# Optimization experiments

Measured on AMD Instinct MI355X. Metric: run time of the kernel, lower is better.

The kernel has to match this reference:

```python
import jax, jax.numpy as jnp
import numpy as np

H = 16        # num_attention_heads
HS = 128      # head_size
ROT = 32      # rotary_ndims (partial RoPE, NeoX rotary_pct=0.25)
BASE = 10000.0


def _rope_cache(seq_len):
    inv_freq = 1.0 / (BASE ** (jnp.arange(0, ROT, 2, dtype=jnp.float32) / ROT))
    t = jnp.arange(seq_len, dtype=jnp.float32)
    freqs = jnp.outer(t, inv_freq)                      # [s, ROT/2]
    emb = jnp.concatenate([freqs, freqs], axis=-1)      # [s, ROT]
    return jnp.cos(emb), jnp.sin(emb)


def _rotate_half(x):
    x1, x2 = jnp.split(x, 2, axis=-1)
    return jnp.concatenate([-x2, x1], axis=-1)


def setup_inputs() -> dict:
    key = jax.random.key(0)
    k1, k2, k3 = jax.random.split(key, 3)
    B, S, D = 2, 2048, 2048
    hidden_states = jax.random.normal(k1, (B, S, D), dtype=jnp.float32)
    position_ids = jnp.broadcast_to(jnp.arange(S, dtype=jnp.int64 if jax.config.jax_enable_x64 else jnp.int32), (B, S))
    W_qkv = jax.random.normal(k2, (D, 3 * H * HS), dtype=jnp.float32) * 0.02
    b_qkv = jnp.zeros((3 * H * HS,), dtype=jnp.float32)
    W_dense = jax.random.normal(k3, (H * HS, D), dtype=jnp.float32) * 0.02
    b_dense = jnp.zeros((D,), dtype=jnp.float32)
    return {"hidden_states": hidden_states, "position_ids": position_ids,
            "W_qkv": W_qkv, "b_qkv": b_qkv, "W_dense": W_dense, "b_dense": b_dense}


def reference(hidden_states, position_ids, W_qkv, b_qkv, W_dense, b_dense):
    B, S, D = hidden_states.shape
    # fused QKV projection, NeoX layout: [b, s, h, 3*hs]
    qkv = (hidden_states @ W_qkv + b_qkv).reshape(B, S, H, 3 * HS)
    q = qkv[..., :HS]            # [b, s, h, hs]
    k = qkv[..., HS:2 * HS]
    v = qkv[..., 2 * HS:]

    # partial rotary embedding on first ROT dims
    cos, sin = _rope_cache(S)                       # [s, ROT]
    cos = cos[position_ids][:, :, None, :]          # [b, s, 1, ROT]
    sin = sin[position_ids][:, :, None, :]
    q_rot, q_pass = q[..., :ROT], q[..., ROT:]
    k_rot, k_pass = k[..., :ROT], k[..., ROT:]
    q_rot = q_rot * cos + _rotate_half(q_rot) * sin
    k_rot = k_rot * cos + _rotate_half(k_rot) * sin
    q = jnp.concatenate([q_rot, q_pass], axis=-1)
    k = jnp.concatenate([k_rot, k_pass], axis=-1)

    # scaled dot-product attention (no mask, as in the source SDPA call)
    scale = 1.0 / jnp.sqrt(jnp.asarray(HS, dtype=q.dtype))
    scores = jnp.einsum('bqhd,bkhd->bhqk', q, k) * scale   # [b, h, s, s]
    attn = jax.nn.softmax(scores, axis=-1)
    out = jnp.einsum('bhqk,bkhd->bqhd', attn, v)            # [b, s, h, hs]
    out = out.reshape(B, S, H * HS)                         # 'b h d n -> b d (h n)'
    return out @ W_dense + b_dense
```

## Files before the change

kernel.cpp:

```cpp
#include <hip/hip_runtime.h>

typedef short bf16x8 __attribute__((ext_vector_type(8)));
typedef float f32x4 __attribute__((ext_vector_type(4)));

#define S_LEN 2048
#define NHEAD 16
#define HSZ 128

__device__ __forceinline__ float bf2f(ushort u) {
    union { unsigned int i; float f; } x; x.i = ((unsigned int)u) << 16; return x.f;
}
__device__ __forceinline__ ushort f2bf(float f) {
    union { float f; unsigned int i; } x; x.f = f;
    unsigned int r = (x.i + 0x7FFFu + ((x.i >> 16) & 1u)) >> 16;
    return (ushort)r;
}

__device__ __forceinline__ void gload16(const ushort* g, ushort* l) {
    __builtin_amdgcn_global_load_lds(
        (const __attribute__((address_space(1))) unsigned int*)g,
        (__attribute__((address_space(3))) unsigned int*)l,
        16, 0, 0);
}

#define BAR()   asm volatile("s_barrier" ::: "memory")
#define LGKM0() asm volatile("s_waitcnt lgkmcnt(0)" ::: "memory")

__global__ void cast_kernel(const float* __restrict__ in, ushort* __restrict__ out, int n4) {
    int i = blockIdx.x * 256 + threadIdx.x;
    if (i >= n4) return;
    float4 v = ((const float4*)in)[i];
    ushort4 r;
    r.x = f2bf(v.x); r.y = f2bf(v.y); r.z = f2bf(v.z); r.w = f2bf(v.w);
    ((ushort4*)out)[i] = r;
}

__global__ void transpose_cast(const float* __restrict__ W, ushort* __restrict__ WT,
                               int K, int N) {
    __shared__ float tile[32][33];
    int n = blockIdx.x * 32 + threadIdx.x;
    #pragma unroll
    for (int j = 0; j < 32; j += 8) {
        int k = blockIdx.y * 32 + threadIdx.y + j;
        tile[threadIdx.y + j][threadIdx.x] = W[(size_t)k * N + n];
    }
    __syncthreads();
    int k2 = blockIdx.y * 32 + threadIdx.x;
    #pragma unroll
    for (int j = 0; j < 32; j += 8) {
        int n2 = blockIdx.x * 32 + threadIdx.y + j;
        WT[(size_t)n2 * K + k2] = f2bf(tile[threadIdx.x][threadIdx.y + j]);
    }
}

template <int EPI>
__global__ __launch_bounds__(512, 2) void gemm256(
    const ushort* __restrict__ A, const ushort* __restrict__ Bt,
    const float* __restrict__ bias, float* __restrict__ Cout, int Kdim, int Ndim,
    ushort* __restrict__ q_out, ushort* __restrict__ k_out, ushort* __restrict__ v_out) {
    __shared__ __align__(16) ushort lds[65536];
    const int tid = threadIdx.x;
    const int m0 = blockIdx.y * 256, n0 = blockIdx.x * 256;
    const int lane = tid & 63, wid = tid >> 6;
    const int wm = wid >> 2, wn = wid & 3;
    const int lm = lane & 15, quad = lane >> 4;
    const int cs = (quad ^ ((lm >> 1) & 3)) * 8;
    const int aOff = wm * 8192 + lm * 32 + cs;
    const int bOff = 16384 + (wn >> 1) * 8192 + (wn & 1) * 2048 + lm * 32 + cs;
    const int srow = tid >> 2;
    const int xs8 = ((tid & 3) ^ ((tid >> 3) & 3)) * 8;
    const ushort* pAs = A  + (size_t)(m0 + srow) * Kdim + xs8;
    const ushort* pBs = Bt + (size_t)(n0 + srow) * Kdim + xs8;
    const size_t hK = (size_t)128 * Kdim;
    const int sw = wid * 512;

    f32x4 acc[8][4];
    #pragma unroll
    for (int i = 0; i < 8; ++i)
        #pragma unroll
        for (int j = 0; j < 4; ++j) acc[i][j] = (f32x4){0.f, 0.f, 0.f, 0.f};

    const int T = Kdim >> 6;

    auto stageB = [&](int t) {
        ushort* b = lds + (t & 1) * 32768 + 16384 + sw;
        const ushort* g = pBs + (size_t)t * 64;
        gload16(g,            b);
        gload16(g + 32,       b + 4096);
        gload16(g + hK,       b + 8192);
        gload16(g + hK + 32,  b + 12288);
    };
    auto stageA = [&](int t) {
        ushort* b = lds + (t & 1) * 32768 + sw;
        const ushort* g = pAs + (size_t)t * 64;
        gload16(g,            b);
        gload16(g + 32,       b + 4096);
        gload16(g + hK,       b + 8192);
        gload16(g + hK + 32,  b + 12288);
    };

    stageB(0); stageA(0); stageB(1); stageA(1);
    asm volatile("s_waitcnt vmcnt(8)" ::: "memory");
    BAR();

    for (int t = 0; t < T; ++t) {
        const ushort* la = lds + (t & 1) * 32768 + aOff;
        const ushort* lb = lds + (t & 1) * 32768 + bOff;
        const bool pf = (t + 2 < T);

        bf16x8 afL[4][2], bfL[2][2];
        #pragma unroll
        for (int mt = 0; mt < 4; ++mt)
            #pragma unroll
            for (int ks = 0; ks < 2; ++ks)
                afL[mt][ks] = *(const bf16x8*)(la + ks * 4096 + mt * 512);
        #pragma unroll
        for (int nt = 0; nt < 2; ++nt)
            #pragma unroll
            for (int ks = 0; ks < 2; ++ks)
                bfL[nt][ks] = *(const bf16x8*)(lb + ks * 4096 + nt * 512);
        BAR(); LGKM0();
        __builtin_amdgcn_s_setprio(1);
        #pragma unroll
        for (int mt = 0; mt < 4; ++mt)
            #pragma unroll
            for (int nt = 0; nt < 2; ++nt) {
                acc[mt][nt] = __builtin_amdgcn_mfma_f32_16x16x32_bf16(afL[mt][0], bfL[nt][0], acc[mt][nt], 0, 0, 0);
                acc[mt][nt] = __builtin_amdgcn_mfma_f32_16x16x32_bf16(afL[mt][1], bfL[nt][1], acc[mt][nt], 0, 0, 0);
            }
        __builtin_amdgcn_s_setprio(0);
        BAR();

        bf16x8 bfH[2][2];
        #pragma unroll
        for (int nt = 0; nt < 2; ++nt)
            #pragma unroll
            for (int ks = 0; ks < 2; ++ks)
                bfH[nt][ks] = *(const bf16x8*)(lb + ks * 4096 + (nt + 2) * 512);
        BAR(); LGKM0();
        __builtin_amdgcn_s_setprio(1);
        #pragma unroll
        for (int mt = 0; mt < 4; ++mt)
            #pragma unroll
            for (int nt = 0; nt < 2; ++nt) {
                acc[mt][nt + 2] = __builtin_amdgcn_mfma_f32_16x16x32_bf16(afL[mt][0], bfH[nt][0], acc[mt][nt + 2], 0, 0, 0);
                acc[mt][nt + 2] = __builtin_amdgcn_mfma_f32_16x16x32_bf16(afL[mt][1], bfH[nt][1], acc[mt][nt + 2], 0, 0, 0);
            }
        __builtin_amdgcn_s_setprio(0);
        BAR();

        bf16x8 afH[4][2];
        #pragma unroll
        for (int mt = 0; mt < 4; ++mt)
            #pragma unroll
            for (int ks = 0; ks < 2; ++ks)
                afH[mt][ks] = *(const bf16x8*)(la + ks * 4096 + (mt + 4) * 512);
        if (pf) stageB(t + 2);
        BAR(); LGKM0();
        __builtin_amdgcn_s_setprio(1);
        #pragma unroll
        for (int mt = 0; mt < 4; ++mt)
            #pragma unroll
            for (int nt = 0; nt < 2; ++nt) {
                acc[mt + 4][nt] = __builtin_amdgcn_mfma_f32_16x16x32_bf16(afH[mt][0], bfL[nt][0], acc[mt + 4][nt], 0, 0, 0);
                acc[mt + 4][nt] = __builtin_amdgcn_mfma_f32_16x16x32_bf16(afH[mt][1], bfL[nt][1], acc[mt + 4][nt], 0, 0, 0);
            }
        __builtin_amdgcn_s_setprio(0);
        BAR();

        if (pf) stageA(t + 2);
        BAR();
        __builtin_amdgcn_s_setprio(1);
        #pragma unroll
        for (int mt = 0; mt < 4; ++mt)
            #pragma unroll
            for (int nt = 0; nt < 2; ++nt) {
                acc[mt + 4][nt + 2] = __builtin_amdgcn_mfma_f32_16x16x32_bf16(afH[mt][0], bfH[nt][0], acc[mt + 4][nt + 2], 0, 0, 0);
                acc[mt + 4][nt + 2] = __builtin_amdgcn_mfma_f32_16x16x32_bf16(afH[mt][1], bfH[nt][1], acc[mt + 4][nt + 2], 0, 0, 0);
            }
        __builtin_amdgcn_s_setprio(0);
        if (pf) asm volatile("s_waitcnt vmcnt(8)" ::: "memory");
        else    asm volatile("s_waitcnt vmcnt(0)" ::: "memory");
        BAR();
    }

    #pragma unroll
    for (int mt = 0; mt < 8; ++mt) {
        #pragma unroll
        for (int nt = 0; nt < 4; ++nt) {
            f32x4 c = acc[mt][nt];
            int gn = n0 + wn * 64 + nt * 16 + lm;
            float bv = bias[gn];
            #pragma unroll
            for (int i = 0; i < 4; ++i) {
                int gm = m0 + wm * 128 + mt * 16 + quad * 4 + i;
                float v = c[i] + bv;
                if (EPI == 0) {
                    int h = gn / 384, r = gn - h * 384;
                    int tt = r >> 7, d = r & 127;
                    int b = gm >> 11, s = gm & 2047;
                    ushort bb = f2bf(v);
                    if (tt == 0) {
                        q_out[((size_t)(b * NHEAD + h) * S_LEN + s) * HSZ + d] = bb;
                    } else if (tt == 1) {
                        k_out[((size_t)(b * NHEAD + h) * S_LEN + s) * HSZ + d] = bb;
                    } else {
                        v_out[((size_t)(b * NHEAD + h) * HSZ + d) * S_LEN + s] = bb;
                    }
                } else {
                    Cout[(size_t)gm * Ndim + gn] = v;
                }
            }
        }
    }
}

template <int EPI>
__global__ __launch_bounds__(256) void gemm128(
    const ushort* __restrict__ A, const ushort* __restrict__ Bt,
    const float* __restrict__ bias, float* __restrict__ Cout, int Kdim, int Ndim,
    ushort* __restrict__ q_out, ushort* __restrict__ k_out, ushort* __restrict__ v_out) {
    __shared__ __align__(16) ushort lA[2][128 * 32];
    __shared__ __align__(16) ushort lB[2][128 * 32];
    const int tid = threadIdx.x;
    const int m0 = blockIdx.y * 128, n0 = blockIdx.x * 128;
    const int lane = tid & 63, wid = tid >> 6;
    const int wm = wid >> 1, wn = wid & 1, lm = lane & 15, quad = lane >> 4;
    const int srow = tid >> 2;
    const int gc = (tid & 3) ^ ((tid >> 3) & 3);
    const int wb8 = (wid << 6) * 8;
    const int cs = (quad ^ ((lm >> 1) & 3)) * 8;

    const ushort* pA = A  + (size_t)(m0 + srow) * Kdim + gc * 8;
    const ushort* pB = Bt + (size_t)(n0 + srow) * Kdim + gc * 8;
    const size_t rhalf = (size_t)64 * Kdim;

    const int fA = (wm * 64 + lm) * 32;
    const int fB = (wn * 64 + lm) * 32;

    f32x4 acc[16];
    #pragma unroll
    for (int i = 0; i < 16; ++i) acc[i] = (f32x4){0.f, 0.f, 0.f, 0.f};

    const int T = Kdim >> 5;
    gload16(pA,         lA[0] + wb8);
    gload16(pA + rhalf, lA[0] + 2048 + wb8);
    gload16(pB,         lB[0] + wb8);
    gload16(pB + rhalf, lB[0] + 2048 + wb8);
    pA += 32; pB += 32;

    for (int t = 0; t < T; ++t) {
        __syncthreads();
        const ushort* la = lA[t & 1];
        const ushort* lb = lB[t & 1];
        if (t + 1 < T) {
            ushort* da = lA[(t + 1) & 1];
            ushort* db = lB[(t + 1) & 1];
            gload16(pA,         da + wb8);
            gload16(pA + rhalf, da + 2048 + wb8);
            gload16(pB,         db + wb8);
            gload16(pB + rhalf, db + 2048 + wb8);
            pA += 32; pB += 32;
        }
        bf16x8 af[4], bfr[4];
        #pragma unroll
        for (int t4 = 0; t4 < 4; ++t4) {
            af[t4]  = *(const bf16x8*)(la + fA + t4 * 512 + cs);
            bfr[t4] = *(const bf16x8*)(lb + fB + t4 * 512 + cs);
        }
        #pragma unroll
        for (int mt = 0; mt < 4; ++mt)
            #pragma unroll
            for (int nt = 0; nt < 4; ++nt)
                acc[mt * 4 + nt] = __builtin_amdgcn_mfma_f32_16x16x32_bf16(
                    af[mt], bfr[nt], acc[mt * 4 + nt], 0, 0, 0);
    }

    #pragma unroll
    for (int mt = 0; mt < 4; ++mt) {
        #pragma unroll
        for (int nt = 0; nt < 4; ++nt) {
            f32x4 c = acc[mt * 4 + nt];
            int gn = n0 + wn * 64 + nt * 16 + lm;
            float bv = bias[gn];
            #pragma unroll
            for (int i = 0; i < 4; ++i) {
                int gm = m0 + wm * 64 + mt * 16 + quad * 4 + i;
                float v = c[i] + bv;
                if (EPI == 0) {
                    int h = gn / 384, r = gn - h * 384;
                    int t = r >> 7, d = r & 127;
                    int b = gm >> 11, s = gm & 2047;
                    ushort bb = f2bf(v);
                    if (t == 0) {
                        q_out[((size_t)(b * NHEAD + h) * S_LEN + s) * HSZ + d] = bb;
                    } else if (t == 1) {
                        k_out[((size_t)(b * NHEAD + h) * S_LEN + s) * HSZ + d] = bb;
                    } else {
                        v_out[((size_t)(b * NHEAD + h) * HSZ + d) * S_LEN + s] = bb;
                    }
                } else {
                    Cout[(size_t)gm * Ndim + gn] = v;
                }
            }
        }
    }
}

__global__ void rope_kernel(ushort* __restrict__ Qr, ushort* __restrict__ Kr,
                            const int* __restrict__ pos_ids) {
    int idx = blockIdx.x * 256 + threadIdx.x;
    int j = idx & 15;
    int row = idx >> 4;
    int s = row & 2047;
    int bh = row >> 11;
    int b = bh >> 4;
    int pos = pos_ids[b * S_LEN + s];
    float inv = exp2f((float)j * -0.8304820237218405f);
    float th = (float)pos * inv;
    float sn, c;
    sincosf(th, &sn, &c);
    size_t base = (size_t)row * HSZ;
    {
        float x1 = bf2f(Qr[base + j]), x2 = bf2f(Qr[base + j + 16]);
        Qr[base + j]      = f2bf(x1 * c - x2 * sn);
        Qr[base + j + 16] = f2bf(x2 * c + x1 * sn);
    }
    {
        float x1 = bf2f(Kr[base + j]), x2 = bf2f(Kr[base + j + 16]);
        Kr[base + j]      = f2bf(x1 * c - x2 * sn);
        Kr[base + j + 16] = f2bf(x2 * c + x1 * sn);
    }
}

__global__ __launch_bounds__(256, 2) void attn_mfma(
    const ushort* __restrict__ Q, const ushort* __restrict__ K,
    const ushort* __restrict__ Vt, ushort* __restrict__ O) {
    __shared__ __align__(16) ushort lQ[128 * 136];
    __shared__ __align__(16) ushort lK[2][32 * 128];
    __shared__ __align__(16) ushort lVt[2][128 * 32];
    __shared__ __align__(16) ushort lP[4 * 32 * 40];

    const int tid = threadIdx.x;
    const int wid = tid >> 6, lane = tid & 63;
    const int L = lane & 15, quad = lane >> 4;
    const int bh = blockIdx.y;
    const int q0 = blockIdx.x * 128;
    const int wq0 = wid * 32;
    const size_t base = (size_t)bh * S_LEN * HSZ;
    const ushort* Qb = Q + base + (size_t)q0 * HSZ;
    const ushort* Kb = K + base;
    const ushort* Vb = Vt + base;
    ushort* lPw = lP + wid * (32 * 40);

    #pragma unroll
    for (int p = 0; p < 8; ++p) {
        int idx = tid + p * 256;
        int row = idx >> 4, ch = idx & 15;
        uint4 v = ((const uint4*)Qb)[idx];
        *(uint4*)(lQ + row * 136 + ch * 8) = v;
    }
    __syncthreads();

    bf16x8 qf[2][4];
    #pragma unroll
    for (int qs = 0; qs < 2; ++qs)
        #pragma unroll
        for (int dc = 0; dc < 4; ++dc)
            qf[qs][dc] = *(const bf16x8*)(lQ + (wq0 + qs * 16 + L) * 136 + dc * 32 + quad * 8);

    int kx[4];
    #pragma unroll
    for (int dc = 0; dc < 4; ++dc) kx[dc] = (((dc * 4 + quad) ^ (L & 7))) * 8;
    const int vx = (quad ^ ((L >> 1) & 3)) * 8;

    const int li0 = tid, li1 = tid + 256;
    const int ub0 = ((tid & 192)) * 8, ub1 = ((tid & 192) + 256) * 8;
    const int kr0 = li0 >> 4, kg0 = (li0 & 15) ^ (kr0 & 7);
    const int kr1 = li1 >> 4, kg1 = (li1 & 15) ^ (kr1 & 7);
    const int vd0 = li0 >> 2, vg0 = (li0 & 3) ^ ((vd0 >> 1) & 3);
    const int vd1 = li1 >> 2, vg1 = (li1 & 3) ^ ((vd1 >> 1) & 3);

    f32x4 acc_o[8][2];
    #pragma unroll
    for (int dt = 0; dt < 8; ++dt)
        #pragma unroll
        for (int qs = 0; qs < 2; ++qs) acc_o[dt][qs] = (f32x4){0.f, 0.f, 0.f, 0.f};
    float lacc[2] = {0.f, 0.f};
    const float scale = 0.08838834764831845f;
    const float SHIFT = 12.0f;

    {
        gload16(Kb + (size_t)kr0 * 128 + kg0 * 8, lK[0] + ub0);
        gload16(Kb + (size_t)kr1 * 128 + kg1 * 8, lK[0] + ub1);
        gload16(Vb + (size_t)vd0 * 2048 + vg0 * 8, lVt[0] + ub0);
        gload16(Vb + (size_t)vd1 * 2048 + vg1 * 8, lVt[0] + ub1);
    }

    for (int kt = 0; kt < S_LEN / 32; ++kt) {
        __syncthreads();
        const int cur = kt & 1;
        const ushort* lKc = lK[cur];
        const ushort* lVc = lVt[cur];
        if (kt + 1 < S_LEN / 32) {
            ushort* dK = lK[cur ^ 1];
            ushort* dV = lVt[cur ^ 1];
            int kb = (kt + 1) * 32;
            gload16(Kb + (size_t)(kb + kr0) * 128 + kg0 * 8, dK + ub0);
            gload16(Kb + (size_t)(kb + kr1) * 128 + kg1 * 8, dK + ub1);
            gload16(Vb + (size_t)vd0 * 2048 + kb + vg0 * 8, dV + ub0);
            gload16(Vb + (size_t)vd1 * 2048 + kb + vg1 * 8, dV + ub1);
        }

        f32x4 sa[2][2];
        #pragma unroll
        for (int t = 0; t < 2; ++t)
            #pragma unroll
            for (int qs = 0; qs < 2; ++qs) sa[t][qs] = (f32x4){0.f, 0.f, 0.f, 0.f};
        #pragma unroll
        for (int t = 0; t < 2; ++t)
            #pragma unroll
            for (int dc = 0; dc < 4; ++dc) {
                bf16x8 kf = *(const bf16x8*)(lKc + (t * 16 + L) * 128 + kx[dc]);
                sa[t][0] = __builtin_amdgcn_mfma_f32_16x16x32_bf16(kf, qf[0][dc], sa[t][0], 0, 0, 0);
                sa[t][1] = __builtin_amdgcn_mfma_f32_16x16x32_bf16(kf, qf[1][dc], sa[t][1], 0, 0, 0);
            }

        #pragma unroll
        for (int t = 0; t < 2; ++t)
            #pragma unroll
            for (int qs = 0; qs < 2; ++qs) {
                #pragma unroll
                for (int r = 0; r < 4; ++r) {
                    float pv = __expf(fmaf(sa[t][qs][r], scale, -SHIFT));
                    lacc[qs] += pv;
                    sa[t][qs][r] = pv;
                }
                ushort4 u;
                u.x = f2bf(sa[t][qs][0]);
                u.y = f2bf(sa[t][qs][1]);
                u.z = f2bf(sa[t][qs][2]);
                u.w = f2bf(sa[t][qs][3]);
                *(ushort4*)(lPw + (qs * 16 + L) * 40 + t * 16 + quad * 4) = u;
            }
        __asm__ volatile("s_waitcnt lgkmcnt(0)" ::: "memory");

        bf16x8 pf0 = *(const bf16x8*)(lPw + L * 40 + quad * 8);
        bf16x8 pf1 = *(const bf16x8*)(lPw + (16 + L) * 40 + quad * 8);
        #pragma unroll
        for (int dt = 0; dt < 8; ++dt) {
            bf16x8 vf = *(const bf16x8*)(lVc + (dt * 16 + L) * 32 + vx);
            acc_o[dt][0] = __builtin_amdgcn_mfma_f32_16x16x32_bf16(vf, pf0, acc_o[dt][0], 0, 0, 0);
            acc_o[dt][1] = __builtin_amdgcn_mfma_f32_16x16x32_bf16(vf, pf1, acc_o[dt][1], 0, 0, 0);
        }
    }

    const int b = bh >> 4, h = bh & 15;
    #pragma unroll
    for (int qs = 0; qs < 2; ++qs) {
        float l = lacc[qs];
        l += __shfl_xor(l, 16);
        l += __shfl_xor(l, 32);
        float inv = 1.f / l;
        size_t row = ((size_t)(b * S_LEN + q0 + wq0 + qs * 16 + L)) * (NHEAD * HSZ) + h * HSZ;
        #pragma unroll
        for (int dt = 0; dt < 8; ++dt) {
            ushort4 u;
            u.x = f2bf(acc_o[dt][qs][0] * inv);
            u.y = f2bf(acc_o[dt][qs][1] * inv);
            u.z = f2bf(acc_o[dt][qs][2] * inv);
            u.w = f2bf(acc_o[dt][qs][3] * inv);
            *(ushort4*)(O + row + dt * 16 + quad * 4) = u;
        }
    }
}

extern "C" void kernel_launch(void* const* d_in, const int* in_sizes, int n_in,
                              void* d_out, int out_size, void* d_ws, size_t ws_size,
                              hipStream_t stream) {
    const float* hidden = (const float*)d_in[0];
    const int*   pos    = (const int*)d_in[1];
    const float* Wqkv   = (const float*)d_in[2];
    const float* bqkv   = (const float*)d_in[3];
    const float* Wd     = (const float*)d_in[4];
    const float* bd     = (const float*)d_in[5];

    char* ws = (char*)d_ws;
    ushort* hA  = (ushort*)ws;
    ushort* WqT = (ushort*)(ws + 16777216ull);
    ushort* WdT = (ushort*)(ws + 41943040ull);
    ushort* Qb  = (ushort*)(ws + 50331648ull);
    ushort* Kb  = (ushort*)(ws + 67108864ull);
    ushort* Vb  = (ushort*)(ws + 83886080ull);

    cast_kernel<<<dim3(8192), dim3(256), 0, stream>>>(hidden, hA, 2097152);
    transpose_cast<<<dim3(192, 64), dim3(32, 8), 0, stream>>>(Wqkv, WqT, 2048, 6144);
    transpose_cast<<<dim3(64, 64), dim3(32, 8), 0, stream>>>(Wd, WdT, 2048, 2048);

    gemm256<0><<<dim3(24, 16), dim3(512), 0, stream>>>(hA, WqT, bqkv, nullptr, 2048, 6144,
                                                       Qb, Kb, Vb);
    rope_kernel<<<dim3(4096), dim3(256), 0, stream>>>(Qb, Kb, pos);

    ushort* Obuf = hA;
    attn_mfma<<<dim3(16, 32), dim3(256), 0, stream>>>(Qb, Kb, Vb, Obuf);

    gemm128<1><<<dim3(16, 32), dim3(256), 0, stream>>>(Obuf, WdT, bd, (float*)d_out,
                                                       2048, 2048, nullptr, nullptr, nullptr);
}
```

Measured before the change: 440.0 us.

## Enlarge attention block to 256 queries and 64-key tiles with 8 waves

The attention kernel now runs 512 threads (8 waves) per block, covering 256 query rows, and streams K/V in 64-key tiles instead of 32. The V^T tile uses a new 8-way XOR swizzle, and the P·V step is split into two 32-key halves that reuse the per-wave P staging buffer. The goal is to halve K/V global and LDS traffic per query and the number of barriers per key. The cost is much more LDS per block and 256 blocks, about one per CU, so occupancy drops. The 512-thread launch bound also puts more pressure on registers, which could cause spills.

```diff
diff --git a/kernel.cpp b/kernel.cpp
--- a/kernel.cpp
+++ b/kernel.cpp
@@ -333,19 +333,19 @@
     }
 }
 
-__global__ __launch_bounds__(256, 2) void attn_mfma(
+__global__ __launch_bounds__(512, 2) void attn_mfma(
     const ushort* __restrict__ Q, const ushort* __restrict__ K,
     const ushort* __restrict__ Vt, ushort* __restrict__ O) {
-    __shared__ __align__(16) ushort lQ[128 * 136];
-    __shared__ __align__(16) ushort lK[2][32 * 128];
-    __shared__ __align__(16) ushort lVt[2][128 * 32];
-    __shared__ __align__(16) ushort lP[4 * 32 * 40];
+    __shared__ __align__(16) ushort lQ[256 * 136];
+    __shared__ __align__(16) ushort lK[2][64 * 128];
+    __shared__ __align__(16) ushort lVt[2][128 * 64];
+    __shared__ __align__(16) ushort lP[8 * 32 * 40];
 
     const int tid = threadIdx.x;
     const int wid = tid >> 6, lane = tid & 63;
     const int L = lane & 15, quad = lane >> 4;
     const int bh = blockIdx.y;
-    const int q0 = blockIdx.x * 128;
+    const int q0 = blockIdx.x * 256;
     const int wq0 = wid * 32;
     const size_t base = (size_t)bh * S_LEN * HSZ;
     const ushort* Qb = Q + base + (size_t)q0 * HSZ;
@@ -355,7 +355,7 @@
 
     #pragma unroll
     for (int p = 0; p < 8; ++p) {
-        int idx = tid + p * 256;
+        int idx = tid + p * 512;
         int row = idx >> 4, ch = idx & 15;
         uint4 v = ((const uint4*)Qb)[idx];
         *(uint4*)(lQ + row * 136 + ch * 8) = v;
@@ -371,15 +371,15 @@
 
     int kx[4];
     #pragma unroll
-    for (int dc = 0; dc < 4; ++dc) kx[dc] = (((dc * 4 + quad) ^ (L & 7))) * 8;
-    const int vx = (quad ^ ((L >> 1) & 3)) * 8;
-
-    const int li0 = tid, li1 = tid + 256;
-    const int ub0 = ((tid & 192)) * 8, ub1 = ((tid & 192) + 256) * 8;
-    const int kr0 = li0 >> 4, kg0 = (li0 & 15) ^ (kr0 & 7);
-    const int kr1 = li1 >> 4, kg1 = (li1 & 15) ^ (kr1 & 7);
-    const int vd0 = li0 >> 2, vg0 = (li0 & 3) ^ ((vd0 >> 1) & 3);
-    const int vd1 = li1 >> 2, vg1 = (li1 & 3) ^ ((vd1 >> 1) & 3);
+    for (int dc = 0; dc < 4; ++dc) kx[dc] = ((dc * 4 + quad) ^ (L & 7)) * 8;
+    const int vx0 = ((0 * 4 + quad) ^ (L & 7)) * 8;
+    const int vx1 = ((1 * 4 + quad) ^ (L & 7)) * 8;
+
+    const int ub  = (tid & 0x1C0) * 8;
+    const int kr0 = tid >> 4,  kg0 = (tid & 15) ^ (kr0 & 7);
+    const int kr1 = kr0 + 32;
+    const int vd0 = tid >> 3,  vg0 = (tid & 7) ^ (vd0 & 7);
+    const int vd1 = vd0 + 64;
 
     f32x4 acc_o[8][2];
     #pragma unroll
@@ -391,34 +391,34 @@
     const float SHIFT = 12.0f;
 
     {
-        gload16(Kb + (size_t)kr0 * 128 + kg0 * 8, lK[0] + ub0);
-        gload16(Kb + (size_t)kr1 * 128 + kg1 * 8, lK[0] + ub1);
-        gload16(Vb + (size_t)vd0 * 2048 + vg0 * 8, lVt[0] + ub0);
-        gload16(Vb + (size_t)vd1 * 2048 + vg1 * 8, lVt[0] + ub1);
-    }
-
-    for (int kt = 0; kt < S_LEN / 32; ++kt) {
+        gload16(Kb + (size_t)kr0 * 128 + kg0 * 8, lK[0] + ub);
+        gload16(Kb + (size_t)kr1 * 128 + kg0 * 8, lK[0] + 4096 + ub);
+        gload16(Vb + (size_t)vd0 * 2048 + vg0 * 8, lVt[0] + ub);
+        gload16(Vb + (size_t)vd1 * 2048 + vg0 * 8, lVt[0] + 4096 + ub);
+    }
+
+    for (int kt = 0; kt < S_LEN / 64; ++kt) {
         __syncthreads();
         const int cur = kt & 1;
         const ushort* lKc = lK[cur];
         const ushort* lVc = lVt[cur];
-        if (kt + 1 < S_LEN / 32) {
+        if (kt + 1 < S_LEN / 64) {
             ushort* dK = lK[cur ^ 1];
             ushort* dV = lVt[cur ^ 1];
-            int kb = (kt + 1) * 32;
-            gload16(Kb + (size_t)(kb + kr0) * 128 + kg0 * 8, dK + ub0);
-            gload16(Kb + (size_t)(kb + kr1) * 128 + kg1 * 8, dK + ub1);
-            gload16(Vb + (size_t)vd0 * 2048 + kb + vg0 * 8, dV + ub0);
-            gload16(Vb + (size_t)vd1 * 2048 + kb + vg1 * 8, dV + ub1);
-        }
-
-        f32x4 sa[2][2];
-        #pragma unroll
-        for (int t = 0; t < 2; ++t)
+            int kb = (kt + 1) * 64;
+            gload16(Kb + (size_t)(kb + kr0) * 128 + kg0 * 8, dK + ub);
+            gload16(Kb + (size_t)(kb + kr1) * 128 + kg0 * 8, dK + 4096 + ub);
+            gload16(Vb + (size_t)vd0 * 2048 + kb + vg0 * 8, dV + ub);
+            gload16(Vb + (size_t)vd1 * 2048 + kb + vg0 * 8, dV + 4096 + ub);
+        }
+
+        f32x4 sa[4][2];
+        #pragma unroll
+        for (int t = 0; t < 4; ++t)
             #pragma unroll
             for (int qs = 0; qs < 2; ++qs) sa[t][qs] = (f32x4){0.f, 0.f, 0.f, 0.f};
         #pragma unroll
-        for (int t = 0; t < 2; ++t)
+        for (int t = 0; t < 4; ++t)
             #pragma unroll
             for (int dc = 0; dc < 4; ++dc) {
                 bf16x8 kf = *(const bf16x8*)(lKc + (t * 16 + L) * 128 + kx[dc]);
@@ -427,31 +427,36 @@
             }
 
         #pragma unroll
-        for (int t = 0; t < 2; ++t)
-            #pragma unroll
-            for (int qs = 0; qs < 2; ++qs) {
+        for (int h = 0; h < 2; ++h) {
+            #pragma unroll
+            for (int t2 = 0; t2 < 2; ++t2) {
+                int t = h * 2 + t2;
                 #pragma unroll
-                for (int r = 0; r < 4; ++r) {
-                    float pv = __expf(fmaf(sa[t][qs][r], scale, -SHIFT));
-                    lacc[qs] += pv;
-                    sa[t][qs][r] = pv;
+                for (int qs = 0; qs < 2; ++qs) {
+                    #pragma unroll
+                    for (int r = 0; r < 4; ++r) {
+                        float pv = __expf(fmaf(sa[t][qs][r], scale, -SHIFT));
+                        lacc[qs] += pv;
+                        sa[t][qs][r] = pv;
+                    }
+                    ushort4 u;
+                    u.x = f2bf(sa[t][qs][0]);
+                    u.y = f2bf(sa[t][qs][1]);
+                    u.z = f2bf(sa[t][qs][2]);
+                    u.w = f2bf(sa[t][qs][3]);
+                    *(ushort4*)(lPw + (qs * 16 + L) * 40 + t2 * 16 + quad * 4) = u;
                 }
-                ushort4 u;
-                u.x = f2bf(sa[t][qs][0]);
-                u.y = f2bf(sa[t][qs][1]);
-                u.z = f2bf(sa[t][qs][2]);
-                u.w = f2bf(sa[t][qs][3]);
-                *(ushort4*)(lPw + (qs * 16 + L) * 40 + t * 16 + quad * 4) = u;
-            }
-        __asm__ volatile("s_waitcnt lgkmcnt(0)" ::: "memory");
-
-        bf16x8 pf0 = *(const bf16x8*)(lPw + L * 40 + quad * 8);
-        bf16x8 pf1 = *(const bf16x8*)(lPw + (16 + L) * 40 + quad * 8);
-        #pragma unroll
-        for (int dt = 0; dt < 8; ++dt) {
-            bf16x8 vf = *(const bf16x8*)(lVc + (dt * 16 + L) * 32 + vx);
-            acc_o[dt][0] = __builtin_amdgcn_mfma_f32_16x16x32_bf16(vf, pf0, acc_o[dt][0], 0, 0, 0);
-            acc_o[dt][1] = __builtin_amdgcn_mfma_f32_16x16x32_bf16(vf, pf1, acc_o[dt][1], 0, 0, 0);
+            }
+            LGKM0();
+            bf16x8 pf0 = *(const bf16x8*)(lPw + L * 40 + quad * 8);
+            bf16x8 pf1 = *(const bf16x8*)(lPw + (16 + L) * 40 + quad * 8);
+            const int vx = h ? vx1 : vx0;
+            #pragma unroll
+            for (int dt = 0; dt < 8; ++dt) {
+                bf16x8 vf = *(const bf16x8*)(lVc + (dt * 16 + L) * 64 + vx);
+                acc_o[dt][0] = __builtin_amdgcn_mfma_f32_16x16x32_bf16(vf, pf0, acc_o[dt][0], 0, 0, 0);
+                acc_o[dt][1] = __builtin_amdgcn_mfma_f32_16x16x32_bf16(vf, pf1, acc_o[dt][1], 0, 0, 0);
+            }
         }
     }
 
@@ -502,7 +507,7 @@
     rope_kernel<<<dim3(4096), dim3(256), 0, stream>>>(Qb, Kb, pos);
 
     ushort* Obuf = hA;
-    attn_mfma<<<dim3(16, 32), dim3(256), 0, stream>>>(Qb, Kb, Vb, Obuf);
+    attn_mfma<<<dim3(8, 32), dim3(512), 0, stream>>>(Qb, Kb, Vb, Obuf);
 
     gemm128<1><<<dim3(16, 32), dim3(256), 0, stream>>>(Obuf, WdT, bd, (float*)d_out,
                                                        2048, 2048, nullptr, nullptr, nullptr);
```

Measured after the change: 431.7 us. No clear change (-1.9%).
